# Optimization experiments

Hardware: AMD Instinct MI355X
Metric: run time of the kernel (lower is better)

Reference implementation:

```python
import jax, jax.numpy as jnp
import numpy as np

HEADS = 16
LN_EPS = 1e-5


def setup_inputs() -> dict:
    key = jax.random.key(0)
    ks = jax.random.split(key, 4)
    B, S, C, U = 2, 2048, 1024, 1024
    scale = 1.0 / np.sqrt(C)
    return {
        "inputs": jax.random.normal(ks[0], (B, S, C), dtype=jnp.float32),
        "Wq": jax.random.normal(ks[1], (C, U), dtype=jnp.float32) * scale,
        "bq": jnp.zeros((U,), dtype=jnp.float32),
        "Wk": jax.random.normal(ks[2], (C, U), dtype=jnp.float32) * scale,
        "bk": jnp.zeros((U,), dtype=jnp.float32),
        "Wv": jax.random.normal(ks[3], (C, U), dtype=jnp.float32) * scale,
        "bv": jnp.zeros((U,), dtype=jnp.float32),
        "ln_gamma": jnp.ones((S, U), dtype=jnp.float32),
        "ln_beta": jnp.zeros((S, U), dtype=jnp.float32),
    }


def reference(inputs, Wq, bq, Wk, bk, Wv, bv, ln_gamma, ln_beta):
    B, S, C = inputs.shape
    U = Wq.shape[1]
    H = HEADS
    dh = U // H

    Q = inputs @ Wq + bq  # [B,S,U]
    K = inputs @ Wk + bk
    V = inputs @ Wv + bv

    # torch: concat(split(X, U//H, dim=-1), dim=0) -> head-major stacking on batch
    def split_heads(X):
        return jnp.moveaxis(X.reshape(B, S, H, dh), 2, 0).reshape(H * B, S, dh)

    Q_, K_, V_ = split_heads(Q), split_heads(K), split_heads(V)

    scores = jnp.einsum('bqd,bkd->bqk', Q_, K_) / jnp.sqrt(jnp.float32(dh))
    tri = jnp.tril(jnp.ones((S, S), dtype=bool))  # causal mask
    scores = jnp.where(tri[None, :, :], scores, jnp.float32(-1e9))
    attn = jax.nn.softmax(scores, axis=-1)
    out_ = jnp.einsum('bqk,bkd->bqd', attn, V_)  # [H*B,S,dh]

    # inverse: split on batch into H chunks of size B, concat on feature dim
    out = jnp.moveaxis(out_.reshape(H, B, S, dh), 0, 2).reshape(B, S, U)

    out = out + inputs  # residual

    # LayerNorm over normalized_shape=[S, U] (joint seq+feature stats)
    mu = jnp.mean(out, axis=(-2, -1), keepdims=True)
    var = jnp.mean(jnp.square(out - mu), axis=(-2, -1), keepdims=True)
    out = (out - mu) / jnp.sqrt(var + LN_EPS) * ln_gamma + ln_beta
    return out
```

## Files before the change

### kernel.cpp

```cpp
#include <hip/hip_runtime.h>
#include <hip/hip_bf16.h>


typedef __bf16 bf16_t;
typedef __bf16 bf16x8 __attribute__((ext_vector_type(8)));
typedef __bf16 bf16x4 __attribute__((ext_vector_type(4)));
typedef _Float16 f16_t;
typedef _Float16 f16x2 __attribute__((ext_vector_type(2)));
typedef _Float16 f16x4 __attribute__((ext_vector_type(4)));
typedef _Float16 f16x8 __attribute__((ext_vector_type(8)));
typedef float f32x4 __attribute__((ext_vector_type(4)));

constexpr int Bsz = 2;
constexpr int Seq = 2048;
constexpr int Cdim = 1024;
constexpr int Udim = 1024;
constexpr int Hn = 16;
constexpr int Dh = 64;
constexpr int Mrows = Bsz * Seq;
constexpr int PerBatch = Seq * Udim;
constexpr float SCLQ = 0.125f * 1.44269504088896340736f;

#if __has_builtin(__builtin_amdgcn_exp2f)
#define EXP2F(x) __builtin_amdgcn_exp2f(x)
#else
#define EXP2F(x) exp2f(x)
#endif

#define AINL __attribute__((always_inline))

__device__ __forceinline__ void gload16(const void* g, void* l)
{
    __builtin_amdgcn_global_load_lds(
        (const __attribute__((address_space(1))) void*)g,
        (__attribute__((address_space(3))) void*)l, 16, 0, 0);
}

__device__ __forceinline__ f16x2 pkrtz(float a, float b)
{
    return __builtin_bit_cast(f16x2, __builtin_amdgcn_cvt_pkrtz(a, b));
}

__global__ __launch_bounds__(256)
void prep(const float* __restrict__ X,
          const float* __restrict__ Wq, const float* __restrict__ Wk,
          const float* __restrict__ Wv,
          bf16_t* __restrict__ Xb,
          bf16_t* __restrict__ Tq, bf16_t* __restrict__ Tk,
          bf16_t* __restrict__ Tv, float* __restrict__ stats)
{
    int z = blockIdx.z;
    int tid = threadIdx.x;
    if (z < 3) {
        const float* W = (z == 0) ? Wq : (z == 1) ? Wk : Wv;
        bf16_t* T = (z == 0) ? Tq : (z == 1) ? Tk : Tv;
        __shared__ bf16_t t[64][65];
        int x0 = blockIdx.x * 64, y0 = blockIdx.y * 64;
        int tx = tid & 63, ty = tid >> 6;
        for (int i = ty; i < 64; i += 4)
            t[i][tx] = (bf16_t)W[(size_t)(y0 + i) * Cdim + x0 + tx];
        __syncthreads();
        for (int i = ty; i < 64; i += 4)
            T[(size_t)(x0 + i) * Cdim + y0 + tx] = t[tx][i];
    } else {
        int bi = blockIdx.y * 16 + blockIdx.x;
        if (bi == 0 && tid < 4) stats[tid] = 0.0f;
        const float4* Xv = (const float4*)X;
#pragma unroll
        for (int k = 0; k < 16; k++) {
            int i = bi * 4096 + k * 256 + tid;
            float4 v = Xv[i];
            bf16x4 o = { (bf16_t)v.x, (bf16_t)v.y, (bf16_t)v.z, (bf16_t)v.w };
            *(bf16x4*)(Xb + (size_t)i * 4) = o;
        }
    }
}

__global__ __launch_bounds__(256)
void gemm_qkv(const bf16_t* __restrict__ X,
              const bf16_t* __restrict__ Wt0, const bf16_t* __restrict__ Wt1,
              const bf16_t* __restrict__ Wt2,
              const float* __restrict__ b0, const float* __restrict__ b1,
              const float* __restrict__ b2,
              f16_t* __restrict__ O0, f16_t* __restrict__ O1, f16_t* __restrict__ O2v)
{
    int z = blockIdx.z;
    const bf16_t* Wt = (z == 0) ? Wt0 : (z == 1) ? Wt1 : Wt2;
    const float* bias = (z == 0) ? b0 : (z == 1) ? b1 : b2;
    float scl = (z == 0) ? SCLQ : 1.0f;

    constexpr int Kd = 1024, Nd = 1024;
    __shared__ __align__(16) bf16_t As[128 * 32];
    __shared__ __align__(16) bf16_t Bs[128 * 32];

    int tid = threadIdx.x;
    int wave = tid >> 6, lane = tid & 63, quad = lane >> 4, l16 = lane & 15;
    int wm = (wave & 1) * 64, wn = (wave >> 1) * 64;
    int m0 = blockIdx.y * 128, n0 = blockIdx.x * 128;

    f32x4 acc[4][4] = {};

    int e0 = wave * 512 + lane * 8;
    int r0 = e0 >> 5, c0 = e0 & 31;
    int e1 = e0 + 2048;
    int r1 = e1 >> 5, c1 = e1 & 31;
    const bf16_t* Ag = X + (size_t)m0 * Kd;
    const bf16_t* Bg = Wt + (size_t)n0 * Kd;
    bf16_t* AsW0 = As + wave * 512;
    bf16_t* AsW1 = As + 2048 + wave * 512;
    bf16_t* BsW0 = Bs + wave * 512;
    bf16_t* BsW1 = Bs + 2048 + wave * 512;

    for (int k0 = 0; k0 < Kd; k0 += 32) {
        gload16(Ag + (size_t)r0 * Kd + k0 + c0, AsW0);
        gload16(Ag + (size_t)r1 * Kd + k0 + c1, AsW1);
        gload16(Bg + (size_t)r0 * Kd + k0 + c0, BsW0);
        gload16(Bg + (size_t)r1 * Kd + k0 + c1, BsW1);
        __syncthreads();

        bf16x8 af[4], bfr[4];
#pragma unroll
        for (int i = 0; i < 4; i++)
            af[i] = *(const bf16x8*)&As[(wm + i * 16 + l16) * 32 + quad * 8];
#pragma unroll
        for (int i = 0; i < 4; i++)
            bfr[i] = *(const bf16x8*)&Bs[(wn + i * 16 + l16) * 32 + quad * 8];
#pragma unroll
        for (int mt = 0; mt < 4; mt++)
#pragma unroll
            for (int nt = 0; nt < 4; nt++)
                acc[mt][nt] = __builtin_amdgcn_mfma_f32_16x16x32_bf16(
                    af[mt], bfr[nt], acc[mt][nt], 0, 0, 0);
        __syncthreads();
    }

    if (z < 2) {
        f16_t* Og = (z == 0) ? O0 : O1;
#pragma unroll
        for (int nt = 0; nt < 4; nt++) {
            int col = n0 + wn + nt * 16 + l16;
            float bv = bias[col];
#pragma unroll
            for (int mt = 0; mt < 4; mt++) {
                int row = m0 + wm + mt * 16 + quad * 4;
#pragma unroll
                for (int r = 0; r < 4; r++)
                    Og[(size_t)(row + r) * Nd + col] = (f16_t)((acc[mt][nt][r] + bv) * scl);
            }
        }
    } else {
        int bb = m0 >> 11;
#pragma unroll
        for (int nt = 0; nt < 4; nt++) {
            int col = n0 + wn + nt * 16 + l16;
            float bv = bias[col];
            int h = col >> 6, d = col & 63;
            f16_t* vbase = O2v + (((size_t)(bb * Hn + h) * Dh + d) << 11);
#pragma unroll
            for (int mt = 0; mt < 4; mt++) {
                int row = m0 + wm + mt * 16 + quad * 4;
                int s = row & (Seq - 1);
                f16x4 pk;
#pragma unroll
                for (int r = 0; r < 4; r++) pk[r] = (f16_t)(acc[mt][nt][r] + bv);
                *(f16x4*)(vbase + s) = pk;
            }
        }
    }
}

__global__ __launch_bounds__(256)
void attn9(const f16_t* __restrict__ Q, const f16_t* __restrict__ K,
           const f16_t* __restrict__ Vt, const float* __restrict__ X,
           bf16_t* __restrict__ R, float* __restrict__ stats)
{
    int id = blockIdx.x;
    int c = id & 7;
    int r = id >> 3;
    int g = r & 3;
    int pi = r >> 2;
    int bh = (g << 3) | c;
    int b = bh >> 4, h = bh & 15;
    int qa = 31 - pi;
    int qb = pi;

    int tid = threadIdx.x;
    int w = tid >> 6, lane = tid & 63, quad = lane >> 4, l16 = lane & 15;
    size_t bS = (size_t)b * Seq;

    __shared__ __align__(16) f16_t Ks[2][4096];
    __shared__ __align__(16) f16_t Vs[2][4096];

    const f16_t* Kg = K + bS * Udim + h * Dh;
    const f16_t* Vg = Vt + ((size_t)(b * Hn + h)) * Dh * Seq;

    int srow = w * 8 + (lane >> 3);
    int schunk = (lane & 7) ^ ((lane >> 3) & 7);
    const f16_t* kp0 = Kg + (size_t)srow * Udim + schunk * 8;
    const f16_t* kp1 = kp0 + (size_t)32 * Udim;
    const f16_t* vp0 = Vg + (size_t)srow * Seq + schunk * 8;
    const f16_t* vp1 = vp0 + (size_t)32 * Seq;

    int qidxA = qa * 64 + w * 16 + l16;
    int qidxB = qb * 64 + w * 16 + l16;
    const f16_t* QpA = Q + (bS + qidxA) * Udim + h * Dh;
    const f16_t* QpB = Q + (bS + qidxB) * Udim + h * Dh;
    f16x8 qfA[2], qfB[2];
#pragma unroll
    for (int s = 0; s < 2; s++) {
        qfA[s] = *(const f16x8*)(QpA + s * 32 + quad * 8);
        qfB[s] = *(const f16x8*)(QpB + s * 32 + quad * 8);
    }

    int m = l16 & 7;
    int kO0 = l16 * 64 + ((quad ^ m) << 3);
    int kO1 = l16 * 64 + (((4 + quad) ^ m) << 3);
    int vO[4];
#pragma unroll
    for (int t = 0; t < 4; t++)
        vO[t] = l16 * 64 + (((t * 32 + quad * 8) ^ (m << 4)) >> 1);

    f32x4 OA[4] = {}, OB[4] = {};
    float lsA = 0.0f, lsB = 0.0f;

    auto STAGE = [&](int nb) AINL {
        gload16(kp0, &Ks[nb][w * 512]);
        gload16(kp1, &Ks[nb][2048 + w * 512]);
        gload16(vp0, &Vs[nb][w * 512]);
        gload16(vp1, &Vs[nb][2048 + w * 512]);
        kp0 += (size_t)64 * Udim; kp1 += (size_t)64 * Udim;
        vp0 += 64; vp1 += 64;
    };

    auto TILE = [&](int buf, bool withB) AINL {
        STAGE(buf ^ 1);
        f32x4 stA[4], stB[4];
#pragma unroll
        for (int t = 0; t < 4; t++) {
            f16x8 kf0 = *(const f16x8*)&Ks[buf][kO0 + t * 1024];
            f16x8 kf1 = *(const f16x8*)&Ks[buf][kO1 + t * 1024];
            f32x4 a = {};
            a = __builtin_amdgcn_mfma_f32_16x16x32_f16(kf0, qfA[0], a, 0, 0, 0);
            a = __builtin_amdgcn_mfma_f32_16x16x32_f16(kf1, qfA[1], a, 0, 0, 0);
            stA[t] = a;
            if (withB) {
                f32x4 bb = {};
                bb = __builtin_amdgcn_mfma_f32_16x16x32_f16(kf0, qfB[0], bb, 0, 0, 0);
                bb = __builtin_amdgcn_mfma_f32_16x16x32_f16(kf1, qfB[1], bb, 0, 0, 0);
                stB[t] = bb;
            }
        }
        f16x4 pA[4], pB[4];
#pragma unroll
        for (int t = 0; t < 4; t++) {
            float p0 = EXP2F(stA[t][0]);
            float p1 = EXP2F(stA[t][1]);
            float p2 = EXP2F(stA[t][2]);
            float p3 = EXP2F(stA[t][3]);
            lsA += (p0 + p1) + (p2 + p3);
            f16x2 lo = pkrtz(p0, p1);
            f16x2 hi = pkrtz(p2, p3);
            pA[t][0] = lo[0]; pA[t][1] = lo[1];
            pA[t][2] = hi[0]; pA[t][3] = hi[1];
            if (withB) {
                float b0 = EXP2F(stB[t][0]);
                float b1 = EXP2F(stB[t][1]);
                float b2 = EXP2F(stB[t][2]);
                float b3 = EXP2F(stB[t][3]);
                lsB += (b0 + b1) + (b2 + b3);
                f16x2 blo = pkrtz(b0, b1);
                f16x2 bhi = pkrtz(b2, b3);
                pB[t][0] = blo[0]; pB[t][1] = blo[1];
                pB[t][2] = bhi[0]; pB[t][3] = bhi[1];
            }
        }
#pragma unroll
        for (int t = 0; t < 4; t++) {
#pragma unroll
            for (int dt = 0; dt < 4; dt++) {
                f16x4 vf = *(const f16x4*)&Vs[buf][vO[t] + dt * 1024];
                OA[dt] = __builtin_amdgcn_mfma_f32_16x16x16f16(vf, pA[t], OA[dt], 0, 0, 0);
                if (withB)
                    OB[dt] = __builtin_amdgcn_mfma_f32_16x16x16f16(vf, pB[t], OB[dt], 0, 0, 0);
            }
        }
        __syncthreads();
    };

    auto TILE_AdB = [&](int buf) AINL {
        STAGE(buf ^ 1);
        int kv0 = qb * 64;
        f32x4 stA[4];
#pragma unroll
        for (int t = 0; t < 4; t++) {
            f16x8 kf0 = *(const f16x8*)&Ks[buf][kO0 + t * 1024];
            f16x8 kf1 = *(const f16x8*)&Ks[buf][kO1 + t * 1024];
            f32x4 a = {};
            a = __builtin_amdgcn_mfma_f32_16x16x32_f16(kf0, qfA[0], a, 0, 0, 0);
            a = __builtin_amdgcn_mfma_f32_16x16x32_f16(kf1, qfA[1], a, 0, 0, 0);
            stA[t] = a;
            if (t <= w) {
                f32x4 bb = {};
                bb = __builtin_amdgcn_mfma_f32_16x16x32_f16(kf0, qfB[0], bb, 0, 0, 0);
                bb = __builtin_amdgcn_mfma_f32_16x16x32_f16(kf1, qfB[1], bb, 0, 0, 0);
                f16x4 pfd;
#pragma unroll
                for (int rr = 0; rr < 4; rr++) {
                    float sv = bb[rr];
                    if (kv0 + t * 16 + quad * 4 + rr > qidxB) sv = -1e30f;
                    float pv = EXP2F(sv);
                    lsB += pv;
                    pfd[rr] = (f16_t)pv;
                }
#pragma unroll
                for (int dt = 0; dt < 4; dt++) {
                    f16x4 vf = *(const f16x4*)&Vs[buf][vO[t] + dt * 1024];
                    OB[dt] = __builtin_amdgcn_mfma_f32_16x16x16f16(vf, pfd, OB[dt], 0, 0, 0);
                }
            }
        }
        f16x4 pA[4];
#pragma unroll
        for (int t = 0; t < 4; t++) {
            float p0 = EXP2F(stA[t][0]);
            float p1 = EXP2F(stA[t][1]);
            float p2 = EXP2F(stA[t][2]);
            float p3 = EXP2F(stA[t][3]);
            lsA += (p0 + p1) + (p2 + p3);
            f16x2 lo = pkrtz(p0, p1);
            f16x2 hi = pkrtz(p2, p3);
            pA[t][0] = lo[0]; pA[t][1] = lo[1];
            pA[t][2] = hi[0]; pA[t][3] = hi[1];
        }
#pragma unroll
        for (int t = 0; t < 4; t++) {
#pragma unroll
            for (int dt = 0; dt < 4; dt++) {
                f16x4 vf = *(const f16x4*)&Vs[buf][vO[t] + dt * 1024];
                OA[dt] = __builtin_amdgcn_mfma_f32_16x16x16f16(vf, pA[t], OA[dt], 0, 0, 0);
            }
        }
        __syncthreads();
    };

    auto DIAG_A = [&](int buf) AINL {
        int kv0 = qa * 64;
#pragma unroll
        for (int t = 0; t < 4; t++) {
            if (t <= w) {
                f16x8 kf0 = *(const f16x8*)&Ks[buf][kO0 + t * 1024];
                f16x8 kf1 = *(const f16x8*)&Ks[buf][kO1 + t * 1024];
                f32x4 a = {};
                a = __builtin_amdgcn_mfma_f32_16x16x32_f16(kf0, qfA[0], a, 0, 0, 0);
                a = __builtin_amdgcn_mfma_f32_16x16x32_f16(kf1, qfA[1], a, 0, 0, 0);
                f16x4 pfd;
#pragma unroll
                for (int rr = 0; rr < 4; rr++) {
                    float sv = a[rr];
                    if (kv0 + t * 16 + quad * 4 + rr > qidxA) sv = -1e30f;
                    float pv = EXP2F(sv);
                    lsA += pv;
                    pfd[rr] = (f16_t)pv;
                }
#pragma unroll
                for (int dt = 0; dt < 4; dt++) {
                    f16x4 vf = *(const f16x4*)&Vs[buf][vO[t] + dt * 1024];
                    OA[dt] = __builtin_amdgcn_mfma_f32_16x16x16f16(vf, pfd, OA[dt], 0, 0, 0);
                }
            }
        }
    };

    STAGE(0);
    __syncthreads();

    {
        int t = 0;
        for (; t + 2 <= qb; t += 2) { TILE(0, true); TILE(1, true); }
        if (t < qb) { TILE(0, true); }
    }
    if (qb & 1) TILE_AdB(1); else TILE_AdB(0);
    {
        int t = qb + 1;
        if ((t & 1) && t < qa) { TILE(1, false); t++; }
        for (; t + 2 <= qa; t += 2) { TILE(0, false); TILE(1, false); }
        if (t < qa) { TILE(0, false); }
    }
    if (qa & 1) DIAG_A(1); else DIAG_A(0);

    lsA += __shfl_xor(lsA, 16);
    lsA += __shfl_xor(lsA, 32);
    lsB += __shfl_xor(lsB, 16);
    lsB += __shfl_xor(lsB, 32);
    float invA = 1.0f / lsA;
    float invB = 1.0f / lsB;

    float s_acc = 0.0f, ss_acc = 0.0f;

    const float* XpA = X + (bS + qidxA) * Udim + h * Dh;
    bf16_t* RpA = R + (bS + qidxA) * Udim + h * Dh;
#pragma unroll
    for (int dt = 0; dt < 4; dt++) {
        f32x4 xv = *(const f32x4*)(XpA + dt * 16 + quad * 4);
        f32x4 o = OA[dt] * invA + xv;
        bf16x4 ob;
#pragma unroll
        for (int rr = 0; rr < 4; rr++) {
            ob[rr] = (bf16_t)o[rr];
            s_acc += o[rr];
            ss_acc += o[rr] * o[rr];
        }
        *(bf16x4*)(RpA + dt * 16 + quad * 4) = ob;
    }

    const float* XpB = X + (bS + qidxB) * Udim + h * Dh;
    bf16_t* RpB = R + (bS + qidxB) * Udim + h * Dh;
#pragma unroll
    for (int dt = 0; dt < 4; dt++) {
        f32x4 xv = *(const f32x4*)(XpB + dt * 16 + quad * 4);
        f32x4 o = OB[dt] * invB + xv;
        bf16x4 ob;
#pragma unroll
        for (int rr = 0; rr < 4; rr++) {
            ob[rr] = (bf16_t)o[rr];
            s_acc += o[rr];
            ss_acc += o[rr] * o[rr];
        }
        *(bf16x4*)(RpB + dt * 16 + quad * 4) = ob;
    }

#pragma unroll
    for (int o = 1; o < 64; o <<= 1) {
        s_acc += __shfl_xor(s_acc, o);
        ss_acc += __shfl_xor(ss_acc, o);
    }
    __shared__ float red[8];
    if (lane == 0) { red[w] = s_acc; red[4 + w] = ss_acc; }
    __syncthreads();
    if (tid == 0) {
        atomicAdd(&stats[b], red[0] + red[1] + red[2] + red[3]);
        atomicAdd(&stats[2 + b], red[4] + red[5] + red[6] + red[7]);
    }
}

__global__ __launch_bounds__(256)
void ln_norm(const bf16_t* __restrict__ R, const float* __restrict__ gamma,
             const float* __restrict__ beta, const float* __restrict__ stats,
             float* __restrict__ out)
{
    constexpr float invN = 1.0f / (float)PerBatch;
    float mu[2], inv[2];
#pragma unroll
    for (int b = 0; b < 2; b++) {
        float m = stats[b] * invN;
        float var = stats[2 + b] * invN - m * m;
        mu[b] = m;
        inv[b] = rsqrtf(var + 1e-5f);
    }
    int i = blockIdx.x * 256 + threadIdx.x;
    int f = i * 8;
    int b = f >> 21;
    int su = f & (PerBatch - 1);
    bf16x8 rv = *(const bf16x8*)(R + f);
    float4 g0 = *(const float4*)(gamma + su);
    float4 g1 = *(const float4*)(gamma + su + 4);
    float4 be0 = *(const float4*)(beta + su);
    float4 be1 = *(const float4*)(beta + su + 4);
    float4 o0, o1;
    o0.x = ((float)rv[0] - mu[b]) * inv[b] * g0.x + be0.x;
    o0.y = ((float)rv[1] - mu[b]) * inv[b] * g0.y + be0.y;
    o0.z = ((float)rv[2] - mu[b]) * inv[b] * g0.z + be0.z;
    o0.w = ((float)rv[3] - mu[b]) * inv[b] * g0.w + be0.w;
    o1.x = ((float)rv[4] - mu[b]) * inv[b] * g1.x + be1.x;
    o1.y = ((float)rv[5] - mu[b]) * inv[b] * g1.y + be1.y;
    o1.z = ((float)rv[6] - mu[b]) * inv[b] * g1.z + be1.z;
    o1.w = ((float)rv[7] - mu[b]) * inv[b] * g1.w + be1.w;
    *(float4*)(out + f) = o0;
    *(float4*)(out + f + 4) = o1;
}

extern "C" void kernel_launch(void* const* d_in, const int* in_sizes, int n_in,
                              void* d_out, int out_size, void* d_ws, size_t ws_size,
                              hipStream_t stream)
{
    const float* X     = (const float*)d_in[0];
    const float* Wq    = (const float*)d_in[1];
    const float* bq    = (const float*)d_in[2];
    const float* Wk    = (const float*)d_in[3];
    const float* bk    = (const float*)d_in[4];
    const float* Wv    = (const float*)d_in[5];
    const float* bv    = (const float*)d_in[6];
    const float* gamma = (const float*)d_in[7];
    const float* beta  = (const float*)d_in[8];
    float* out = (float*)d_out;

    char* ws = (char*)d_ws;
    size_t off = 0;
    auto alloc = [&](size_t bytes) -> void* {
        void* p = ws + off;
        off += (bytes + 255) & ~(size_t)255;
        return p;
    };
    bf16_t* Xb = (bf16_t*)alloc((size_t)Mrows * Cdim * 2);
    bf16_t* Tq = (bf16_t*)alloc((size_t)Cdim * Udim * 2);
    bf16_t* Tk = (bf16_t*)alloc((size_t)Cdim * Udim * 2);
    bf16_t* Tv = (bf16_t*)alloc((size_t)Cdim * Udim * 2);
    f16_t*  Qb = (f16_t*)alloc((size_t)Mrows * Udim * 2);
    f16_t*  Kb = (f16_t*)alloc((size_t)Mrows * Udim * 2);
    f16_t*  Vtb = (f16_t*)alloc((size_t)Mrows * Udim * 2);
    bf16_t* Rb = (bf16_t*)alloc((size_t)Mrows * Udim * 2);
    float*  stats = (float*)alloc(4 * sizeof(float));

    prep<<<dim3(16, 16, 4), 256, 0, stream>>>(X, Wq, Wk, Wv, Xb, Tq, Tk, Tv, stats);
    gemm_qkv<<<dim3(8, 32, 3), 256, 0, stream>>>(Xb, Tq, Tk, Tv, bq, bk, bv, Qb, Kb, Vtb);
    attn9<<<dim3(512), 256, 0, stream>>>(Qb, Kb, Vtb, X, Rb, stats);
    ln_norm<<<dim3(2048), 256, 0, stream>>>(Rb, gamma, beta, stats, out);
}
```

Measured before the change: 186.3 us.

## Split attention KV range across two blocks with partial-sum merge via flags

Each causal query-tile pair is now handled by two blocks that each take half of the 33 KV tiles, doubling the grid from 512 to 1024 blocks. Partial O accumulators and row sums are written to workspace, and whichever block arrives second (detected through an atomic flag) merges them and does the residual and stats epilogue. The aim is more parallelism and better load balance on the attention kernel. The cost is extra global traffic for the partials, fences and atomics, and a reshuffled workspace layout where POA overlaps the Xb/Tq region.

```diff
diff --git a/kernel.cpp b/kernel.cpp
--- a/kernel.cpp
+++ b/kernel.cpp
@@ -47,7 +47,8 @@
           const float* __restrict__ Wv,
           bf16_t* __restrict__ Xb,
           bf16_t* __restrict__ Tq, bf16_t* __restrict__ Tk,
-          bf16_t* __restrict__ Tv, float* __restrict__ stats)
+          bf16_t* __restrict__ Tv, float* __restrict__ stats,
+          int* __restrict__ flags)
 {
     int z = blockIdx.z;
     int tid = threadIdx.x;
@@ -64,7 +65,11 @@
             T[(size_t)(x0 + i) * Cdim + y0 + tx] = t[tx][i];
     } else {
         int bi = blockIdx.y * 16 + blockIdx.x;
-        if (bi == 0 && tid < 4) stats[tid] = 0.0f;
+        if (bi == 0) {
+            if (tid < 4) stats[tid] = 0.0f;
+            flags[tid] = 0;
+            flags[tid + 256] = 0;
+        }
         const float4* Xv = (const float4*)X;
 #pragma unroll
         for (int k = 0; k < 16; k++) {
@@ -169,20 +174,26 @@
     }
 }
 
-__global__ __launch_bounds__(256)
-void attn9(const f16_t* __restrict__ Q, const f16_t* __restrict__ K,
-           const f16_t* __restrict__ Vt, const float* __restrict__ X,
-           bf16_t* __restrict__ R, float* __restrict__ stats)
+__global__ __launch_bounds__(256, 4)
+void attn10(const f16_t* __restrict__ Q, const f16_t* __restrict__ K,
+            const f16_t* __restrict__ Vt, const float* __restrict__ X,
+            bf16_t* __restrict__ R, float* __restrict__ stats,
+            float* __restrict__ POA, float* __restrict__ PLS,
+            int* __restrict__ flags)
 {
     int id = blockIdx.x;
     int c = id & 7;
     int r = id >> 3;
-    int g = r & 3;
-    int pi = r >> 2;
+    int s = r & 1;
+    int rr = r >> 1;
+    int g = rr & 3;
+    int pi = rr >> 2;
     int bh = (g << 3) | c;
     int b = bh >> 4, h = bh & 15;
     int qa = 31 - pi;
     int qb = pi;
+    int split = 15 - pi;
+    int pg = bh * 16 + pi;
 
     int tid = threadIdx.x;
     int w = tid >> 6, lane = tid & 63, quad = lane >> 4, l16 = lane & 15;
@@ -190,26 +201,32 @@
 
     __shared__ __align__(16) f16_t Ks[2][4096];
     __shared__ __align__(16) f16_t Vs[2][4096];
+    __shared__ float red[8];
+    __shared__ int shOld;
 
     const f16_t* Kg = K + bS * Udim + h * Dh;
     const f16_t* Vg = Vt + ((size_t)(b * Hn + h)) * Dh * Seq;
 
     int srow = w * 8 + (lane >> 3);
     int schunk = (lane & 7) ^ ((lane >> 3) & 7);
-    const f16_t* kp0 = Kg + (size_t)srow * Udim + schunk * 8;
+    int t0 = (s == 0) ? 0 : split;
+    const f16_t* kp0 = Kg + (size_t)(t0 * 64 + srow) * Udim + schunk * 8;
     const f16_t* kp1 = kp0 + (size_t)32 * Udim;
-    const f16_t* vp0 = Vg + (size_t)srow * Seq + schunk * 8;
+    const f16_t* vp0 = Vg + (size_t)srow * Seq + t0 * 64 + schunk * 8;
     const f16_t* vp1 = vp0 + (size_t)32 * Seq;
 
     int qidxA = qa * 64 + w * 16 + l16;
     int qidxB = qb * 64 + w * 16 + l16;
     const f16_t* QpA = Q + (bS + qidxA) * Udim + h * Dh;
-    const f16_t* QpB = Q + (bS + qidxB) * Udim + h * Dh;
     f16x8 qfA[2], qfB[2];
 #pragma unroll
-    for (int s = 0; s < 2; s++) {
-        qfA[s] = *(const f16x8*)(QpA + s * 32 + quad * 8);
-        qfB[s] = *(const f16x8*)(QpB + s * 32 + quad * 8);
+    for (int ss = 0; ss < 2; ss++)
+        qfA[ss] = *(const f16x8*)(QpA + ss * 32 + quad * 8);
+    if (s == 0) {
+        const f16_t* QpB = Q + (bS + qidxB) * Udim + h * Dh;
+#pragma unroll
+        for (int ss = 0; ss < 2; ss++)
+            qfB[ss] = *(const f16x8*)(QpB + ss * 32 + quad * 8);
     }
 
     int m = l16 & 7;
@@ -232,18 +249,20 @@
         vp0 += 64; vp1 += 64;
     };
 
-    auto TILE = [&](int buf, bool withB) AINL {
+    auto TILE = [&](int buf, bool wA, bool wB) AINL {
         STAGE(buf ^ 1);
         f32x4 stA[4], stB[4];
 #pragma unroll
         for (int t = 0; t < 4; t++) {
             f16x8 kf0 = *(const f16x8*)&Ks[buf][kO0 + t * 1024];
             f16x8 kf1 = *(const f16x8*)&Ks[buf][kO1 + t * 1024];
-            f32x4 a = {};
-            a = __builtin_amdgcn_mfma_f32_16x16x32_f16(kf0, qfA[0], a, 0, 0, 0);
-            a = __builtin_amdgcn_mfma_f32_16x16x32_f16(kf1, qfA[1], a, 0, 0, 0);
-            stA[t] = a;
-            if (withB) {
+            if (wA) {
+                f32x4 a = {};
+                a = __builtin_amdgcn_mfma_f32_16x16x32_f16(kf0, qfA[0], a, 0, 0, 0);
+                a = __builtin_amdgcn_mfma_f32_16x16x32_f16(kf1, qfA[1], a, 0, 0, 0);
+                stA[t] = a;
+            }
+            if (wB) {
                 f32x4 bb = {};
                 bb = __builtin_amdgcn_mfma_f32_16x16x32_f16(kf0, qfB[0], bb, 0, 0, 0);
                 bb = __builtin_amdgcn_mfma_f32_16x16x32_f16(kf1, qfB[1], bb, 0, 0, 0);
@@ -253,16 +272,18 @@
         f16x4 pA[4], pB[4];
 #pragma unroll
         for (int t = 0; t < 4; t++) {
-            float p0 = EXP2F(stA[t][0]);
-            float p1 = EXP2F(stA[t][1]);
-            float p2 = EXP2F(stA[t][2]);
-            float p3 = EXP2F(stA[t][3]);
-            lsA += (p0 + p1) + (p2 + p3);
-            f16x2 lo = pkrtz(p0, p1);
-            f16x2 hi = pkrtz(p2, p3);
-            pA[t][0] = lo[0]; pA[t][1] = lo[1];
-            pA[t][2] = hi[0]; pA[t][3] = hi[1];
-            if (withB) {
+            if (wA) {
+                float p0 = EXP2F(stA[t][0]);
+                float p1 = EXP2F(stA[t][1]);
+                float p2 = EXP2F(stA[t][2]);
+                float p3 = EXP2F(stA[t][3]);
+                lsA += (p0 + p1) + (p2 + p3);
+                f16x2 lo = pkrtz(p0, p1);
+                f16x2 hi = pkrtz(p2, p3);
+                pA[t][0] = lo[0]; pA[t][1] = lo[1];
+                pA[t][2] = hi[0]; pA[t][3] = hi[1];
+            }
+            if (wB) {
                 float b0 = EXP2F(stB[t][0]);
                 float b1 = EXP2F(stB[t][1]);
                 float b2 = EXP2F(stB[t][2]);
@@ -279,8 +300,9 @@
 #pragma unroll
             for (int dt = 0; dt < 4; dt++) {
                 f16x4 vf = *(const f16x4*)&Vs[buf][vO[t] + dt * 1024];
-                OA[dt] = __builtin_amdgcn_mfma_f32_16x16x16f16(vf, pA[t], OA[dt], 0, 0, 0);
-                if (withB)
+                if (wA)
+                    OA[dt] = __builtin_amdgcn_mfma_f32_16x16x16f16(vf, pA[t], OA[dt], 0, 0, 0);
+                if (wB)
                     OB[dt] = __builtin_amdgcn_mfma_f32_16x16x16f16(vf, pB[t], OB[dt], 0, 0, 0);
             }
         }
@@ -305,12 +327,12 @@
                 bb = __builtin_amdgcn_mfma_f32_16x16x32_f16(kf1, qfB[1], bb, 0, 0, 0);
                 f16x4 pfd;
 #pragma unroll
-                for (int rr = 0; rr < 4; rr++) {
-                    float sv = bb[rr];
-                    if (kv0 + t * 16 + quad * 4 + rr > qidxB) sv = -1e30f;
+                for (int rr2 = 0; rr2 < 4; rr2++) {
+                    float sv = bb[rr2];
+                    if (kv0 + t * 16 + quad * 4 + rr2 > qidxB) sv = -1e30f;
                     float pv = EXP2F(sv);
                     lsB += pv;
-                    pfd[rr] = (f16_t)pv;
+                    pfd[rr2] = (f16_t)pv;
                 }
 #pragma unroll
                 for (int dt = 0; dt < 4; dt++) {
@@ -343,6 +365,34 @@
         __syncthreads();
     };
 
+    auto BDIAG = [&](int buf) AINL {
+        int kv0 = qb * 64;
+#pragma unroll
+        for (int t = 0; t < 4; t++) {
+            if (t <= w) {
+                f16x8 kf0 = *(const f16x8*)&Ks[buf][kO0 + t * 1024];
+                f16x8 kf1 = *(const f16x8*)&Ks[buf][kO1 + t * 1024];
+                f32x4 bb = {};
+                bb = __builtin_amdgcn_mfma_f32_16x16x32_f16(kf0, qfB[0], bb, 0, 0, 0);
+                bb = __builtin_amdgcn_mfma_f32_16x16x32_f16(kf1, qfB[1], bb, 0, 0, 0);
+                f16x4 pfd;
+#pragma unroll
+                for (int rr2 = 0; rr2 < 4; rr2++) {
+                    float sv = bb[rr2];
+                    if (kv0 + t * 16 + quad * 4 + rr2 > qidxB) sv = -1e30f;
+                    float pv = EXP2F(sv);
+                    lsB += pv;
+                    pfd[rr2] = (f16_t)pv;
+                }
+#pragma unroll
+                for (int dt = 0; dt < 4; dt++) {
+                    f16x4 vf = *(const f16x4*)&Vs[buf][vO[t] + dt * 1024];
+                    OB[dt] = __builtin_amdgcn_mfma_f32_16x16x16f16(vf, pfd, OB[dt], 0, 0, 0);
+                }
+            }
+        }
+    };
+
     auto DIAG_A = [&](int buf) AINL {
         int kv0 = qa * 64;
 #pragma unroll
@@ -355,12 +405,12 @@
                 a = __builtin_amdgcn_mfma_f32_16x16x32_f16(kf1, qfA[1], a, 0, 0, 0);
                 f16x4 pfd;
 #pragma unroll
-                for (int rr = 0; rr < 4; rr++) {
-                    float sv = a[rr];
-                    if (kv0 + t * 16 + quad * 4 + rr > qidxA) sv = -1e30f;
+                for (int rr2 = 0; rr2 < 4; rr2++) {
+                    float sv = a[rr2];
+                    if (kv0 + t * 16 + quad * 4 + rr2 > qidxA) sv = -1e30f;
                     float pv = EXP2F(sv);
                     lsA += pv;
-                    pfd[rr] = (f16_t)pv;
+                    pfd[rr2] = (f16_t)pv;
                 }
 #pragma unroll
                 for (int dt = 0; dt < 4; dt++) {
@@ -371,62 +421,96 @@
         }
     };
 
+#define RUNN(n, C0, C1)                                    \
+    do {                                                   \
+        int _n = (n);                                      \
+        if (_n > 0 && par) { C1; _n--; par ^= 1; }         \
+        while (_n >= 2) { C0; C1; _n -= 2; }               \
+        if (_n > 0) { C0; par ^= 1; }                      \
+    } while (0)
+
+    int par = 0;
     STAGE(0);
     __syncthreads();
 
-    {
-        int t = 0;
-        for (; t + 2 <= qb; t += 2) { TILE(0, true); TILE(1, true); }
-        if (t < qb) { TILE(0, true); }
-    }
-    if (qb & 1) TILE_AdB(1); else TILE_AdB(0);
-    {
-        int t = qb + 1;
-        if ((t & 1) && t < qa) { TILE(1, false); t++; }
-        for (; t + 2 <= qa; t += 2) { TILE(0, false); TILE(1, false); }
-        if (t < qa) { TILE(0, false); }
-    }
-    if (qa & 1) DIAG_A(1); else DIAG_A(0);
+    if (s == 0) {
+        int pA = (split < qb) ? split : qb;
+        RUNN(pA, TILE(0, true, true), TILE(1, true, true));
+        if (split > qb) {
+            if (par) TILE_AdB(1); else TILE_AdB(0);
+            par ^= 1;
+            RUNN(split - qb - 1, TILE(0, true, false), TILE(1, true, false));
+        } else {
+            RUNN(qb - split, TILE(0, false, true), TILE(1, false, true));
+            if (par) BDIAG(1); else BDIAG(0);
+        }
+    } else {
+        RUNN(16, TILE(0, true, false), TILE(1, true, false));
+        if (par) DIAG_A(1); else DIAG_A(0);
+    }
+#undef RUNN
+
+    float s_acc = 0.0f, ss_acc = 0.0f;
+
+    if (s == 0) {
+        lsB += __shfl_xor(lsB, 16);
+        lsB += __shfl_xor(lsB, 32);
+        float invB = 1.0f / lsB;
+        const float* XpB = X + (bS + qidxB) * Udim + h * Dh;
+        bf16_t* RpB = R + (bS + qidxB) * Udim + h * Dh;
+#pragma unroll
+        for (int dt = 0; dt < 4; dt++) {
+            f32x4 xv = *(const f32x4*)(XpB + dt * 16 + quad * 4);
+            f32x4 o = OB[dt] * invB + xv;
+            bf16x4 ob;
+#pragma unroll
+            for (int rr2 = 0; rr2 < 4; rr2++) {
+                ob[rr2] = (bf16_t)o[rr2];
+                s_acc += o[rr2];
+                ss_acc += o[rr2] * o[rr2];
+            }
+            *(bf16x4*)(RpB + dt * 16 + quad * 4) = ob;
+        }
+    }
 
     lsA += __shfl_xor(lsA, 16);
     lsA += __shfl_xor(lsA, 32);
-    lsB += __shfl_xor(lsB, 16);
-    lsB += __shfl_xor(lsB, 32);
-    float invA = 1.0f / lsA;
-    float invB = 1.0f / lsB;
-
-    float s_acc = 0.0f, ss_acc = 0.0f;
-
-    const float* XpA = X + (bS + qidxA) * Udim + h * Dh;
-    bf16_t* RpA = R + (bS + qidxA) * Udim + h * Dh;
-#pragma unroll
-    for (int dt = 0; dt < 4; dt++) {
-        f32x4 xv = *(const f32x4*)(XpA + dt * 16 + quad * 4);
-        f32x4 o = OA[dt] * invA + xv;
-        bf16x4 ob;
-#pragma unroll
-        for (int rr = 0; rr < 4; rr++) {
-            ob[rr] = (bf16_t)o[rr];
-            s_acc += o[rr];
-            ss_acc += o[rr] * o[rr];
-        }
-        *(bf16x4*)(RpA + dt * 16 + quad * 4) = ob;
-    }
-
-    const float* XpB = X + (bS + qidxB) * Udim + h * Dh;
-    bf16_t* RpB = R + (bS + qidxB) * Udim + h * Dh;
-#pragma unroll
-    for (int dt = 0; dt < 4; dt++) {
-        f32x4 xv = *(const f32x4*)(XpB + dt * 16 + quad * 4);
-        f32x4 o = OB[dt] * invB + xv;
-        bf16x4 ob;
-#pragma unroll
-        for (int rr = 0; rr < 4; rr++) {
-            ob[rr] = (bf16_t)o[rr];
-            s_acc += o[rr];
-            ss_acc += o[rr] * o[rr];
-        }
-        *(bf16x4*)(RpB + dt * 16 + quad * 4) = ob;
+    {
+        float* slot = POA + (((size_t)pg * 2 + s) << 12) + ((w * 16 + l16) << 6) + quad * 4;
+#pragma unroll
+        for (int dt = 0; dt < 4; dt++)
+            *(f32x4*)(slot + dt * 16) = OA[dt];
+        if (lane < 16)
+            PLS[((size_t)pg * 2 + s) * 64 + w * 16 + l16] = lsA;
+    }
+    __threadfence();
+    __syncthreads();
+    if (tid == 0) shOld = atomicAdd(&flags[pg], 1);
+    __syncthreads();
+
+    if (shOld == 1) {
+        __threadfence();
+        const float* os = POA + (((size_t)pg * 2 + (s ^ 1)) << 12) + ((w * 16 + l16) << 6) + quad * 4;
+#pragma unroll
+        for (int dt = 0; dt < 4; dt++)
+            OA[dt] += *(const f32x4*)(os + dt * 16);
+        lsA += PLS[((size_t)pg * 2 + (s ^ 1)) * 64 + w * 16 + l16];
+        float invA = 1.0f / lsA;
+        const float* XpA = X + (bS + qidxA) * Udim + h * Dh;
+        bf16_t* RpA = R + (bS + qidxA) * Udim + h * Dh;
+#pragma unroll
+        for (int dt = 0; dt < 4; dt++) {
+            f32x4 xv = *(const f32x4*)(XpA + dt * 16 + quad * 4);
+            f32x4 o = OA[dt] * invA + xv;
+            bf16x4 ob;
+#pragma unroll
+            for (int rr2 = 0; rr2 < 4; rr2++) {
+                ob[rr2] = (bf16_t)o[rr2];
+                s_acc += o[rr2];
+                ss_acc += o[rr2] * o[rr2];
+            }
+            *(bf16x4*)(RpA + dt * 16 + quad * 4) = ob;
+        }
     }
 
 #pragma unroll
@@ -434,7 +518,6 @@
         s_acc += __shfl_xor(s_acc, o);
         ss_acc += __shfl_xor(ss_acc, o);
     }
-    __shared__ float red[8];
     if (lane == 0) { red[w] = s_acc; red[4 + w] = ss_acc; }
     __syncthreads();
     if (tid == 0) {
@@ -495,24 +578,22 @@
     float* out = (float*)d_out;
 
     char* ws = (char*)d_ws;
-    size_t off = 0;
-    auto alloc = [&](size_t bytes) -> void* {
-        void* p = ws + off;
-        off += (bytes + 255) & ~(size_t)255;
-        return p;
-    };
-    bf16_t* Xb = (bf16_t*)alloc((size_t)Mrows * Cdim * 2);
-    bf16_t* Tq = (bf16_t*)alloc((size_t)Cdim * Udim * 2);
-    bf16_t* Tk = (bf16_t*)alloc((size_t)Cdim * Udim * 2);
-    bf16_t* Tv = (bf16_t*)alloc((size_t)Cdim * Udim * 2);
-    f16_t*  Qb = (f16_t*)alloc((size_t)Mrows * Udim * 2);
-    f16_t*  Kb = (f16_t*)alloc((size_t)Mrows * Udim * 2);
-    f16_t*  Vtb = (f16_t*)alloc((size_t)Mrows * Udim * 2);
-    bf16_t* Rb = (bf16_t*)alloc((size_t)Mrows * Udim * 2);
-    float*  stats = (float*)alloc(4 * sizeof(float));
-
-    prep<<<dim3(16, 16, 4), 256, 0, stream>>>(X, Wq, Wk, Wv, Xb, Tq, Tk, Tv, stats);
+    constexpr size_t MB = 1024 * 1024;
+    f16_t*  Qb   = (f16_t*)(ws + 0 * MB);
+    f16_t*  Kb   = (f16_t*)(ws + 8 * MB);
+    f16_t*  Vtb  = (f16_t*)(ws + 16 * MB);
+    bf16_t* Rb   = (bf16_t*)(ws + 24 * MB);
+    bf16_t* Xb   = (bf16_t*)(ws + 32 * MB);
+    bf16_t* Tq   = (bf16_t*)(ws + 40 * MB);
+    bf16_t* Tk   = (bf16_t*)(ws + 42 * MB);
+    bf16_t* Tv   = (bf16_t*)(ws + 44 * MB);
+    float*  POA  = (float*)(ws + 32 * MB);
+    float*  PLS  = (float*)(ws + 48 * MB);
+    int*    flags = (int*)(ws + 48 * MB + 256 * 1024);
+    float*  stats = (float*)(ws + 48 * MB + 260 * 1024);
+
+    prep<<<dim3(16, 16, 4), 256, 0, stream>>>(X, Wq, Wk, Wv, Xb, Tq, Tk, Tv, stats, flags);
     gemm_qkv<<<dim3(8, 32, 3), 256, 0, stream>>>(Xb, Tq, Tk, Tv, bq, bk, bv, Qb, Kb, Vtb);
-    attn9<<<dim3(512), 256, 0, stream>>>(Qb, Kb, Vtb, X, Rb, stats);
+    attn10<<<dim3(1024), 256, 0, stream>>>(Qb, Kb, Vtb, X, Rb, stats, POA, PLS, flags);
     ln_norm<<<dim3(2048), 256, 0, stream>>>(Rb, gamma, beta, stats, out);
 }
```

Result: slower. 375.4 us (+101.5%).
